# Performance work log

Measured on AMD Instinct MI355X. Metric: run time of the kernel, lower is better.

The kernel has to match this reference:

```python
import jax, jax.numpy as jnp
import numpy as np

DIM = 768
HEADS = 12
HEAD_DIM = DIM // HEADS
SCALE = HEAD_DIM ** -0.5


def setup_inputs() -> dict:
    key = jax.random.key(0)
    ks = jax.random.split(key, 6)
    B, N, M, C = 4, 2048, 1024, DIM
    x = jax.random.normal(ks[0], (B, N, C), dtype=jnp.float32)
    r = jax.random.normal(ks[1], (B, M, C), dtype=jnp.float32)
    s = 1.0 / np.sqrt(C)
    W_q = jax.random.normal(ks[2], (C, C), dtype=jnp.float32) * s
    W_kv = jax.random.normal(ks[3], (C, 2 * C), dtype=jnp.float32) * s
    W_proj = jax.random.normal(ks[4], (C, C), dtype=jnp.float32) * s
    b_proj = jax.random.normal(ks[5], (C,), dtype=jnp.float32) * 0.02
    return {"x": x, "r": r, "W_q": W_q, "W_kv": W_kv, "W_proj": W_proj, "b_proj": b_proj}


def reference(x, r, W_q, W_kv, W_proj, b_proj):
    B, N, C = x.shape
    _, M, _ = r.shape
    H, D = HEADS, C // HEADS
    # projections (no bias on q/kv per qkv_bias=False)
    q = (x @ W_q).reshape(B, N, H, D)            # bnhd
    kv = (r @ W_kv).reshape(B, M, 2, H, D)
    k = kv[:, :, 0]                               # bmhd
    v = kv[:, :, 1]                               # bmhd
    attn = jnp.einsum('bnhd,bmhd->bhnm', q, k) * SCALE
    attn = jax.nn.softmax(attn, axis=-1)
    out = jnp.einsum('bhnm,bmhd->bnhd', attn, v).reshape(B, N, C)
    return out @ W_proj + b_proj
```

## Files before the change

kernel.cpp:

```cpp
#include <hip/hip_runtime.h>
#include <hip/hip_bf16.h>
#include <cstdint>

#define HEADS 12

typedef __attribute__((ext_vector_type(8))) __bf16 bf16x8;
typedef __attribute__((ext_vector_type(4))) __bf16 bf16x4;
typedef __attribute__((ext_vector_type(4))) float f32x4;
typedef __attribute__((ext_vector_type(16))) float f32x16;

#define AS1 __attribute__((address_space(1)))
#define AS3 __attribute__((address_space(3)))

__device__ __forceinline__ void gload16(const void* src, void* lds) {
  __builtin_amdgcn_global_load_lds((AS1 void*)src, (AS3 void*)lds, 16, 0, 0);
}

__device__ __forceinline__ uint32_t cvtpk(float lo, float hi) {
  uint32_t r;
  asm("v_cvt_pk_bf16_f32 %0, %1, %2" : "=v"(r) : "v"(lo), "v"(hi));
  return r;
}

__device__ __forceinline__ float exp2_fast(float x) {
  float r;
  asm("v_exp_f32 %0, %1" : "=v"(r) : "v"(x));
  return r;
}

__global__ void k_cast2(const float* __restrict__ x, const float* __restrict__ r,
                        __bf16* __restrict__ xb, __bf16* __restrict__ rb) {
  int i = (blockIdx.x * 256 + threadIdx.x) * 4;
  const float* src;
  __bf16* dst;
  int off;
  if (i < 6291456) { src = x; dst = xb; off = i; }
  else             { src = r; dst = rb; off = i - 6291456; }
  float4 v = *(const float4*)(src + off);
  bf16x4 o;
  o[0] = (__bf16)v.x; o[1] = (__bf16)v.y; o[2] = (__bf16)v.z; o[3] = (__bf16)v.w;
  *(bf16x4*)(dst + off) = o;
}

__global__ void k_twc3(const float* __restrict__ Wq, const float* __restrict__ Wkv,
                       const float* __restrict__ Wp, __bf16* __restrict__ wqt,
                       __bf16* __restrict__ wkvt, __bf16* __restrict__ wpt) {
  __shared__ float tile[32][33];
  const float* W; __bf16* Wt; int N; float scale;
  if (blockIdx.z == 0)      { W = Wq;  Wt = wqt;  N = 768;  scale = 0.18033688011112042f; }
  else if (blockIdx.z == 1) { W = Wkv; Wt = wkvt; N = 1536; scale = 1.0f; }
  else                      { W = Wp;  Wt = wpt;  N = 768;  scale = 1.0f; }
  int nt = blockIdx.x, kt = blockIdx.y;
  if (nt * 32 >= N) return;
  int c = threadIdx.x & 31, r0 = threadIdx.x >> 5;
#pragma unroll
  for (int i = 0; i < 4; ++i) {
    int r = r0 + i * 8;
    tile[r][c] = W[(size_t)(kt * 32 + r) * N + nt * 32 + c];
  }
  __syncthreads();
#pragma unroll
  for (int i = 0; i < 4; ++i) {
    int r = r0 + i * 8;
    Wt[(size_t)(nt * 32 + r) * 768 + kt * 32 + c] = (__bf16)(tile[c][r] * scale);
  }
}

__global__ __launch_bounds__(256, 2) void k_gemm12(
    const __bf16* __restrict__ xb, const __bf16* __restrict__ rb,
    const __bf16* __restrict__ wqt, const __bf16* __restrict__ wkvt,
    __bf16* __restrict__ qb, __bf16* __restrict__ kbp, __bf16* __restrict__ vbp) {
  __shared__ __align__(16) char ldsA[2][16384];
  __shared__ __align__(16) char ldsB[2][16384];
  const int tid = threadIdx.x;
  const int ln = tid & 63;
  const int w = tid >> 6;
  int id = blockIdx.x;
  id = (id & 7) * 96 + (id >> 3);
  const __bf16* A; const __bf16* Bt; int bm0, bn0; bool qpart;
  if (id < 384) { A = xb; Bt = wqt;  bm0 = (id / 6) * 128;  bn0 = (id % 6) * 128;  qpart = true; }
  else { int i2 = id - 384; A = rb; Bt = wkvt; bm0 = (i2 / 12) * 128; bn0 = (i2 % 12) * 128; qpart = false; }
  const int wm0 = (w >> 1) * 64, wn0 = (w & 1) * 64;

  auto stage = [&](char* lds, const __bf16* G, int row0, int k0) {
    const char* gb = (const char*)(G + (size_t)row0 * 768 + k0);
#pragma unroll
    for (int c = 0; c < 4; ++c) {
      int off = c * 4096 + tid * 16;
      int row = off >> 7;
      int s = ((off >> 4) & 7) ^ (row & 7);
      gload16(gb + (size_t)row * 1536 + (s << 4), lds + c * 4096 + (w << 10));
    }
  };

  f32x4 acc[4][4] = {};
  stage(ldsA[0], A, bm0, 0);
  stage(ldsB[0], Bt, bn0, 0);
  __syncthreads();
  for (int kt = 0; kt < 12; ++kt) {
    const char* bufA = ldsA[kt & 1];
    const char* bufB = ldsB[kt & 1];
    if (kt + 1 < 12) {
      stage(ldsA[(kt + 1) & 1], A, bm0, (kt + 1) << 6);
      stage(ldsB[(kt + 1) & 1], Bt, bn0, (kt + 1) << 6);
    }
    bf16x8 af[2][4], bf[2][4];
#pragma unroll
    for (int kk = 0; kk < 2; ++kk)
#pragma unroll
      for (int mt = 0; mt < 4; ++mt) {
        int row = wm0 + mt * 16 + (ln & 15);
        af[kk][mt] = *(const bf16x8*)(bufA + row * 128 + (((kk * 4 + (ln >> 4)) ^ (row & 7)) << 4));
      }
#pragma unroll
    for (int kk = 0; kk < 2; ++kk)
#pragma unroll
      for (int nt = 0; nt < 4; ++nt) {
        int row = wn0 + nt * 16 + (ln & 15);
        bf[kk][nt] = *(const bf16x8*)(bufB + row * 128 + (((kk * 4 + (ln >> 4)) ^ (row & 7)) << 4));
      }
    __builtin_amdgcn_s_setprio(1);
#pragma unroll
    for (int kk = 0; kk < 2; ++kk)
#pragma unroll
      for (int mt = 0; mt < 4; ++mt)
#pragma unroll
        for (int nt = 0; nt < 4; ++nt)
          acc[mt][nt] = __builtin_amdgcn_mfma_f32_16x16x32_bf16(af[kk][mt], bf[kk][nt], acc[mt][nt], 0, 0, 0);
    __builtin_amdgcn_s_setprio(0);
    __syncthreads();
  }

  char* ldsT = &ldsA[0][0];
  const bool vpart = (!qpart) && (bn0 >= 768);
  if (!vpart) {
#pragma unroll
    for (int mt = 0; mt < 4; ++mt)
#pragma unroll
      for (int nt = 0; nt < 4; ++nt)
#pragma unroll
        for (int jj = 0; jj < 4; ++jj) {
          int rowl = wm0 + mt * 16 + ((ln >> 4) << 2) + jj;
          int colb = (wn0 + nt * 16 + (ln & 15)) * 2;
          *(__bf16*)(ldsT + rowl * 256 + (colb ^ ((rowl & 7) << 4))) = (__bf16)acc[mt][nt][jj];
        }
  } else {
#pragma unroll
    for (int mt = 0; mt < 4; ++mt)
#pragma unroll
      for (int nt = 0; nt < 4; ++nt)
#pragma unroll
        for (int jj = 0; jj < 4; ++jj) {
          int dloc = wn0 + nt * 16 + (ln & 15);
          int kvb = (wm0 + mt * 16 + ((ln >> 4) << 2) + jj) * 2;
          *(__bf16*)(ldsT + dloc * 256 + (kvb ^ ((dloc & 7) << 4))) = (__bf16)acc[mt][nt][jj];
        }
  }
  __syncthreads();

  if (qpart) {
#pragma unroll
    for (int it = 0; it < 8; ++it) {
      int rowl = it * 16 + (tid >> 4);
      int colb = (tid & 15) * 16;
      bf16x8 v = *(const bf16x8*)(ldsT + rowl * 256 + (colb ^ ((rowl & 7) << 4)));
      *(bf16x8*)(qb + (size_t)(bm0 + rowl) * 768 + bn0 + (tid & 15) * 8) = v;
    }
  } else if (!vpart) {
    const int bb = bm0 >> 10, kvb0 = (bm0 & 1023) >> 5, hh0 = bn0 >> 6;
#pragma unroll
    for (int it = 0; it < 8; ++it) {
      int hh = it >> 2, t32 = it & 3;
      int dc = tid >> 5, kvl = tid & 31;
      int rowl = t32 * 32 + kvl;
      int colb = hh * 128 + (dc >> 1) * 32 + (dc & 1) * 16;
      bf16x8 v = *(const bf16x8*)(ldsT + rowl * 256 + (colb ^ ((rowl & 7) << 4)));
      *(bf16x8*)(kbp + ((size_t)(bb * 12 + hh0 + hh) * 32 + kvb0 + t32) * 2048 + tid * 8) = v;
    }
  } else {
    const int bb = bm0 >> 10, kvb0 = (bm0 & 1023) >> 5, hh0 = (bn0 - 768) >> 6;
#pragma unroll
    for (int it = 0; it < 8; ++it) {
      int hh = it >> 2, t32 = it & 3;
      int d = ((tid >> 7) << 5) + (tid & 31);
      int kvl8 = (((tid >> 6) & 1) << 4) + (((tid >> 5) & 1) << 3);
      int dloc = hh * 64 + d;
      int kvb = (t32 * 32 + kvl8) * 2;
      bf16x8 v = *(const bf16x8*)(ldsT + dloc * 256 + (kvb ^ ((dloc & 7) << 4)));
      *(bf16x8*)(vbp + ((size_t)(bb * 12 + hh0 + hh) * 32 + kvb0 + t32) * 2048 + tid * 8) = v;
    }
  }
}

__global__ __launch_bounds__(256, 2) void k_gemmP(
    const __bf16* __restrict__ A, const __bf16* __restrict__ Bt,
    float* __restrict__ C, const float* __restrict__ bias) {
  __shared__ __align__(16) char ldsA[2][16384];
  __shared__ __align__(16) char ldsB[2][16384];
  const int tid = threadIdx.x;
  const int ln = tid & 63;
  const int w = tid >> 6;
  int bid = blockIdx.y * 6 + blockIdx.x;
  bid = (bid & 7) * 48 + (bid >> 3);
  const int bm0 = (bid / 6) * 128, bn0 = (bid % 6) * 128;
  const int wm0 = (w >> 1) * 64, wn0 = (w & 1) * 64;

  auto stage = [&](char* lds, const __bf16* G, int row0, int k0) {
    const char* gb = (const char*)(G + (size_t)row0 * 768 + k0);
#pragma unroll
    for (int c = 0; c < 4; ++c) {
      int off = c * 4096 + tid * 16;
      int row = off >> 7;
      int s = ((off >> 4) & 7) ^ (row & 7);
      gload16(gb + (size_t)row * 1536 + (s << 4), lds + c * 4096 + (w << 10));
    }
  };

  f32x4 acc[4][4] = {};
  stage(ldsA[0], A, bm0, 0);
  stage(ldsB[0], Bt, bn0, 0);
  __syncthreads();
  for (int kt = 0; kt < 12; ++kt) {
    const char* bufA = ldsA[kt & 1];
    const char* bufB = ldsB[kt & 1];
    if (kt + 1 < 12) {
      stage(ldsA[(kt + 1) & 1], A, bm0, (kt + 1) << 6);
      stage(ldsB[(kt + 1) & 1], Bt, bn0, (kt + 1) << 6);
    }
    bf16x8 af[2][4], bf[2][4];
#pragma unroll
    for (int kk = 0; kk < 2; ++kk)
#pragma unroll
      for (int mt = 0; mt < 4; ++mt) {
        int row = wm0 + mt * 16 + (ln & 15);
        af[kk][mt] = *(const bf16x8*)(bufA + row * 128 + (((kk * 4 + (ln >> 4)) ^ (row & 7)) << 4));
      }
#pragma unroll
    for (int kk = 0; kk < 2; ++kk)
#pragma unroll
      for (int nt = 0; nt < 4; ++nt) {
        int row = wn0 + nt * 16 + (ln & 15);
        bf[kk][nt] = *(const bf16x8*)(bufB + row * 128 + (((kk * 4 + (ln >> 4)) ^ (row & 7)) << 4));
      }
    __builtin_amdgcn_s_setprio(1);
#pragma unroll
    for (int kk = 0; kk < 2; ++kk)
#pragma unroll
      for (int mt = 0; mt < 4; ++mt)
#pragma unroll
        for (int nt = 0; nt < 4; ++nt)
          acc[mt][nt] = __builtin_amdgcn_mfma_f32_16x16x32_bf16(af[kk][mt], bf[kk][nt], acc[mt][nt], 0, 0, 0);
    __builtin_amdgcn_s_setprio(0);
    __syncthreads();
  }
#pragma unroll
  for (int mt = 0; mt < 4; ++mt) {
    int row = bm0 + wm0 + mt * 16 + ((ln >> 4) << 2);
#pragma unroll
    for (int nt = 0; nt < 4; ++nt) {
      int col = bn0 + wn0 + nt * 16 + (ln & 15);
      float bv = bias[col];
#pragma unroll
      for (int jj = 0; jj < 4; ++jj)
        C[(size_t)(row + jj) * 768 + col] = acc[mt][nt][jj] + bv;
    }
  }
}

__global__ __launch_bounds__(256, 3) void k_attn(
    const __bf16* __restrict__ q, const __bf16* __restrict__ kb,
    const __bf16* __restrict__ vb, __bf16* __restrict__ ao) {
  __shared__ __align__(16) char ldsK[3][8192];
  const int tid = threadIdx.x, ln = tid & 63;
  const int l5 = ln >> 5, l32 = ln & 31, w = tid >> 6;
  int id = blockIdx.y * 16 + blockIdx.x;
  id = (id & 7) * 96 + (id >> 3);
  const int qt = id & 15, bh = id >> 4;
  const int b = bh / HEADS, h = bh % HEADS;
  const int qrow = b * 2048 + qt * 128 + w * 32 + l32;

  const char* kbase = (const char*)kb + (size_t)bh * 131072;
  const __bf16* vbase = vb + (size_t)bh * 65536;
  const int vchunk = l5 * 256 + l32 * 8;

  auto stageK = [&](int t, int buf) {
    gload16(kbase + (size_t)t * 8192 + tid * 16, ldsK[buf] + tid * 16);
    gload16(kbase + (size_t)t * 8192 + 4096 + tid * 16, ldsK[buf] + 4096 + tid * 16);
  };

  bf16x8 qf[4];
#pragma unroll
  for (int s = 0; s < 4; ++s)
    qf[s] = *(const bf16x8*)(q + (size_t)qrow * 768 + h * 64 + 16 * s + 8 * l5);

  stageK(0, 0);
  stageK(1, 1);

  f32x16 accO[2] = {};
  float mrow = -1e30f, lrow = 0.f;

  asm volatile("s_waitcnt vmcnt(0)" ::: "memory");
  __builtin_amdgcn_s_barrier();

  for (int t = 0; t < 16; ++t) {
    const char* bufK = ldsK[t % 3];

    bf16x8 vf[2][2][2];
    {
      const __bf16* vt = vbase + (size_t)(2 * t) * 2048 + vchunk;
#pragma unroll
      for (int nt = 0; nt < 2; ++nt)
#pragma unroll
        for (int dt = 0; dt < 2; ++dt)
#pragma unroll
          for (int ks = 0; ks < 2; ++ks)
            vf[nt][dt][ks] = *(const bf16x8*)(vt + nt * 2048 + (dt * 2 + ks) * 512);
    }
    if (t < 14) stageK(t + 2, (t + 2) % 3);

    f32x16 s16[2] = {};
    __builtin_amdgcn_s_setprio(1);
#pragma unroll
    for (int s = 0; s < 4; ++s) {
      bf16x8 kf0 = *(const bf16x8*)(bufK + (s * 2 + l5) * 512 + l32 * 16);
      s16[0] = __builtin_amdgcn_mfma_f32_32x32x16_bf16(kf0, qf[s], s16[0], 0, 0, 0);
      bf16x8 kf1 = *(const bf16x8*)(bufK + 4096 + (s * 2 + l5) * 512 + l32 * 16);
      s16[1] = __builtin_amdgcn_mfma_f32_32x32x16_bf16(kf1, qf[s], s16[1], 0, 0, 0);
    }
    __builtin_amdgcn_s_setprio(0);

    float lm = s16[0][0];
#pragma unroll
    for (int nt = 0; nt < 2; ++nt)
#pragma unroll
      for (int i = 0; i < 16; ++i) lm = fmaxf(lm, s16[nt][i]);
    if (!__all(lm <= mrow + 8.0f)) {
      float mx = fmaxf(lm, __shfl_xor(lm, 32, 64));
      float mn = fmaxf(mrow, mx);
      float corr = exp2_fast(mrow - mn);
      mrow = mn;
      lrow *= corr;
#pragma unroll
      for (int dt = 0; dt < 2; ++dt)
#pragma unroll
        for (int i = 0; i < 16; ++i) accO[dt][i] *= corr;
    }
    float ps = 0.f;
#pragma unroll
    for (int nt = 0; nt < 2; ++nt)
#pragma unroll
      for (int i = 0; i < 16; ++i) {
        float e = exp2_fast(s16[nt][i] - mrow);
        s16[nt][i] = e;
        ps += e;
      }
    lrow += ps;

    bf16x8 pk[2][2];
#pragma unroll
    for (int nt = 0; nt < 2; ++nt) {
      uint32_t c0[4], c1[4];
#pragma unroll
      for (int j = 0; j < 4; ++j) {
        c0[j] = cvtpk(s16[nt][4 * j], s16[nt][4 * j + 1]);
        c1[j] = cvtpk(s16[nt][4 * j + 2], s16[nt][4 * j + 3]);
      }
      uint32_t w00 = c0[0], w02 = c0[1];
      asm("v_permlane32_swap_b32 %0, %1" : "+v"(w00), "+v"(w02));
      uint32_t w01 = c1[0], w03 = c1[1];
      asm("v_permlane32_swap_b32 %0, %1" : "+v"(w01), "+v"(w03));
      uint32_t w10 = c0[2], w12 = c0[3];
      asm("v_permlane32_swap_b32 %0, %1" : "+v"(w10), "+v"(w12));
      uint32_t w11 = c1[2], w13 = c1[3];
      asm("v_permlane32_swap_b32 %0, %1" : "+v"(w11), "+v"(w13));
      union { uint32_t u[4]; bf16x8 v; } pk0, pk1;
      pk0.u[0] = w00; pk0.u[1] = w01; pk0.u[2] = w02; pk0.u[3] = w03;
      pk1.u[0] = w10; pk1.u[1] = w11; pk1.u[2] = w12; pk1.u[3] = w13;
      pk[nt][0] = pk0.v;
      pk[nt][1] = pk1.v;
    }

    __builtin_amdgcn_s_setprio(1);
#pragma unroll
    for (int nt = 0; nt < 2; ++nt)
#pragma unroll
      for (int ks = 0; ks < 2; ++ks) {
        accO[0] = __builtin_amdgcn_mfma_f32_32x32x16_bf16(vf[nt][0][ks], pk[nt][ks], accO[0], 0, 0, 0);
        accO[1] = __builtin_amdgcn_mfma_f32_32x32x16_bf16(vf[nt][1][ks], pk[nt][ks], accO[1], 0, 0, 0);
      }
    __builtin_amdgcn_s_setprio(0);

    __builtin_amdgcn_sched_barrier(0);
    __builtin_amdgcn_s_barrier();
  }

  float l = lrow + __shfl_xor(lrow, 32, 64);
  float inv = 1.0f / l;
  size_t rowb = (size_t)qrow * 768 + h * 64;
#pragma unroll
  for (int dt = 0; dt < 2; ++dt)
#pragma unroll
    for (int j = 0; j < 4; ++j) {
      bf16x4 o;
#pragma unroll
      for (int i = 0; i < 4; ++i) o[i] = (__bf16)(accO[dt][4 * j + i] * inv);
      *(bf16x4*)(ao + rowb + dt * 32 + 8 * j + 4 * l5) = o;
    }
}

extern "C" void kernel_launch(void* const* d_in, const int* in_sizes, int n_in,
                              void* d_out, int out_size, void* d_ws, size_t ws_size,
                              hipStream_t stream) {
  const float* x = (const float*)d_in[0];
  const float* r = (const float*)d_in[1];
  const float* Wq = (const float*)d_in[2];
  const float* Wkv = (const float*)d_in[3];
  const float* Wp = (const float*)d_in[4];
  const float* bp = (const float*)d_in[5];

  char* ws = (char*)d_ws;
  __bf16* xb  = (__bf16*)ws; ws += (size_t)6291456 * 2;
  __bf16* rb  = (__bf16*)ws; ws += (size_t)3145728 * 2;
  __bf16* wqt = (__bf16*)ws; ws += (size_t)589824 * 2;
  __bf16* wkvt= (__bf16*)ws; ws += (size_t)1179648 * 2;
  __bf16* wpt = (__bf16*)ws; ws += (size_t)589824 * 2;
  __bf16* qb  = (__bf16*)ws; ws += (size_t)6291456 * 2;
  __bf16* kbk = (__bf16*)ws; ws += (size_t)3145728 * 2;
  __bf16* vbk = (__bf16*)ws; ws += (size_t)3145728 * 2;
  __bf16* ao  = (__bf16*)ws;

  k_cast2<<<9216, 256, 0, stream>>>(x, r, xb, rb);
  k_twc3<<<dim3(48, 24, 3), 256, 0, stream>>>(Wq, Wkv, Wp, wqt, wkvt, wpt);
  k_gemm12<<<768, 256, 0, stream>>>(xb, rb, wqt, wkvt, qb, kbk, vbk);
  k_attn<<<dim3(16, 48), 256, 0, stream>>>(qb, kbk, vbk, ao);
  k_gemmP<<<dim3(6, 64), 256, 0, stream>>>(ao, wpt, (float*)d_out, bp);
}
```

Baseline: 99.96 us.

## Replace LDS-staged K tiles with per-wave register prefetch in attention

Result: no change. 101.4 us (+1.4%).

```diff
diff --git a/kernel.cpp b/kernel.cpp
--- a/kernel.cpp
+++ b/kernel.cpp
@@ -267,73 +267,68 @@
   }
 }
 
-__global__ __launch_bounds__(256, 3) void k_attn(
+__global__ __launch_bounds__(64, 2) void k_attn(
     const __bf16* __restrict__ q, const __bf16* __restrict__ kb,
     const __bf16* __restrict__ vb, __bf16* __restrict__ ao) {
-  __shared__ __align__(16) char ldsK[3][8192];
-  const int tid = threadIdx.x, ln = tid & 63;
-  const int l5 = ln >> 5, l32 = ln & 31, w = tid >> 6;
-  int id = blockIdx.y * 16 + blockIdx.x;
-  id = (id & 7) * 96 + (id >> 3);
-  const int qt = id & 15, bh = id >> 4;
+  const int ln = threadIdx.x & 63;
+  const int l5 = ln >> 5, l32 = ln & 31;
+  int id = blockIdx.x;
+  id = (id & 7) * 384 + (id >> 3);
+  const int qt = id & 63, bh = id >> 6;
   const int b = bh / HEADS, h = bh % HEADS;
-  const int qrow = b * 2048 + qt * 128 + w * 32 + l32;
+  const int qrow = b * 2048 + qt * 32 + l32;
 
   const char* kbase = (const char*)kb + (size_t)bh * 131072;
   const __bf16* vbase = vb + (size_t)bh * 65536;
   const int vchunk = l5 * 256 + l32 * 8;
 
-  auto stageK = [&](int t, int buf) {
-    gload16(kbase + (size_t)t * 8192 + tid * 16, ldsK[buf] + tid * 16);
-    gload16(kbase + (size_t)t * 8192 + 4096 + tid * 16, ldsK[buf] + 4096 + tid * 16);
-  };
-
   bf16x8 qf[4];
 #pragma unroll
   for (int s = 0; s < 4; ++s)
     qf[s] = *(const bf16x8*)(q + (size_t)qrow * 768 + h * 64 + 16 * s + 8 * l5);
 
-  stageK(0, 0);
-  stageK(1, 1);
+  bf16x8 kc[8], vc[8];
+#pragma unroll
+  for (int s = 0; s < 4; ++s) {
+    kc[2 * s]     = *(const bf16x8*)(kbase + (2 * s + l5) * 512 + l32 * 16);
+    kc[2 * s + 1] = *(const bf16x8*)(kbase + 4096 + (2 * s + l5) * 512 + l32 * 16);
+  }
+#pragma unroll
+  for (int nt = 0; nt < 2; ++nt)
+#pragma unroll
+    for (int dk = 0; dk < 4; ++dk)
+      vc[nt * 4 + dk] = *(const bf16x8*)(vbase + nt * 2048 + dk * 512 + vchunk);
 
   f32x16 accO[2] = {};
   float mrow = -1e30f, lrow = 0.f;
 
-  asm volatile("s_waitcnt vmcnt(0)" ::: "memory");
-  __builtin_amdgcn_s_barrier();
-
+#pragma unroll
   for (int t = 0; t < 16; ++t) {
-    const char* bufK = ldsK[t % 3];
-
-    bf16x8 vf[2][2][2];
-    {
-      const __bf16* vt = vbase + (size_t)(2 * t) * 2048 + vchunk;
-#pragma unroll
-      for (int nt = 0; nt < 2; ++nt)
-#pragma unroll
-        for (int dt = 0; dt < 2; ++dt)
-#pragma unroll
-          for (int ks = 0; ks < 2; ++ks)
-            vf[nt][dt][ks] = *(const bf16x8*)(vt + nt * 2048 + (dt * 2 + ks) * 512);
-    }
-    if (t < 14) stageK(t + 2, (t + 2) % 3);
-
     f32x16 s16[2] = {};
     __builtin_amdgcn_s_setprio(1);
 #pragma unroll
     for (int s = 0; s < 4; ++s) {
-      bf16x8 kf0 = *(const bf16x8*)(bufK + (s * 2 + l5) * 512 + l32 * 16);
-      s16[0] = __builtin_amdgcn_mfma_f32_32x32x16_bf16(kf0, qf[s], s16[0], 0, 0, 0);
-      bf16x8 kf1 = *(const bf16x8*)(bufK + 4096 + (s * 2 + l5) * 512 + l32 * 16);
-      s16[1] = __builtin_amdgcn_mfma_f32_32x32x16_bf16(kf1, qf[s], s16[1], 0, 0, 0);
+      s16[0] = __builtin_amdgcn_mfma_f32_32x32x16_bf16(kc[2 * s], qf[s], s16[0], 0, 0, 0);
+      s16[1] = __builtin_amdgcn_mfma_f32_32x32x16_bf16(kc[2 * s + 1], qf[s], s16[1], 0, 0, 0);
     }
     __builtin_amdgcn_s_setprio(0);
 
-    float lm = s16[0][0];
-#pragma unroll
-    for (int nt = 0; nt < 2; ++nt)
-#pragma unroll
-      for (int i = 0; i < 16; ++i) lm = fmaxf(lm, s16[nt][i]);
+    if (t < 15) {
+      const char* kn = kbase + (size_t)(t + 1) * 8192;
+#pragma unroll
+      for (int s = 0; s < 4; ++s) {
+        kc[2 * s]     = *(const bf16x8*)(kn + (2 * s + l5) * 512 + l32 * 16);
+        kc[2 * s + 1] = *(const bf16x8*)(kn + 4096 + (2 * s + l5) * 512 + l32 * 16);
+      }
+    }
+
+    float m8[8];
+#pragma unroll
+    for (int i = 0; i < 8; ++i)
+      m8[i] = fmaxf(fmaxf(s16[0][i], s16[0][i + 8]), fmaxf(s16[1][i], s16[1][i + 8]));
+    float m4a = fmaxf(m8[0], m8[1]), m4b = fmaxf(m8[2], m8[3]);
+    float m4c = fmaxf(m8[4], m8[5]), m4d = fmaxf(m8[6], m8[7]);
+    float lm = fmaxf(fmaxf(m4a, m4b), fmaxf(m4c, m4d));
     if (!__all(lm <= mrow + 8.0f)) {
       float mx = fmaxf(lm, __shfl_xor(lm, 32, 64));
       float mn = fmaxf(mrow, mx);
@@ -385,13 +380,19 @@
     for (int nt = 0; nt < 2; ++nt)
 #pragma unroll
       for (int ks = 0; ks < 2; ++ks) {
-        accO[0] = __builtin_amdgcn_mfma_f32_32x32x16_bf16(vf[nt][0][ks], pk[nt][ks], accO[0], 0, 0, 0);
-        accO[1] = __builtin_amdgcn_mfma_f32_32x32x16_bf16(vf[nt][1][ks], pk[nt][ks], accO[1], 0, 0, 0);
+        accO[0] = __builtin_amdgcn_mfma_f32_32x32x16_bf16(vc[nt * 4 + ks], pk[nt][ks], accO[0], 0, 0, 0);
+        accO[1] = __builtin_amdgcn_mfma_f32_32x32x16_bf16(vc[nt * 4 + 2 + ks], pk[nt][ks], accO[1], 0, 0, 0);
       }
     __builtin_amdgcn_s_setprio(0);
 
-    __builtin_amdgcn_sched_barrier(0);
-    __builtin_amdgcn_s_barrier();
+    if (t < 15) {
+      const __bf16* vn = vbase + (size_t)(2 * (t + 1)) * 2048 + vchunk;
+#pragma unroll
+      for (int nt = 0; nt < 2; ++nt)
+#pragma unroll
+        for (int dk = 0; dk < 4; ++dk)
+          vc[nt * 4 + dk] = *(const bf16x8*)(vn + nt * 2048 + dk * 512);
+    }
   }
 
   float l = lrow + __shfl_xor(lrow, 32, 64);
@@ -432,6 +433,6 @@
   k_cast2<<<9216, 256, 0, stream>>>(x, r, xb, rb);
   k_twc3<<<dim3(48, 24, 3), 256, 0, stream>>>(Wq, Wkv, Wp, wqt, wkvt, wpt);
   k_gemm12<<<768, 256, 0, stream>>>(xb, rb, wqt, wkvt, qb, kbk, vbk);
-  k_attn<<<dim3(16, 48), 256, 0, stream>>>(qb, kbk, vbk, ao);
+  k_attn<<<3072, 64, 0, stream>>>(qb, kbk, vbk, ao);
   k_gemmP<<<dim3(6, 64), 256, 0, stream>>>(ao, wpt, (float*)d_out, bp);
 }
```
